# Optimization experiments

Measured on AMD Instinct MI355X. Metric: run time of the kernel, lower is better.

The kernel has to match this reference:

```python
import jax, jax.numpy as jnp
import numpy as np

# Active hierarchy constraints from the default 14x14 matrix:
# (2->5), (5->6), (6->7), (8->3)
_I = np.array([2, 5, 6, 8], dtype=np.int32)
_J = np.array([5, 6, 7, 3], dtype=np.int32)
BATCH = 2_000_000
NUM_CLASSES = 14


def setup_inputs() -> dict:
    key = jax.random.key(0)
    k1, = jax.random.split(key, 1)
    predictions = jax.random.uniform(k1, (BATCH, NUM_CLASSES), dtype=jnp.float32)
    return {
        "predictions": predictions,
        "temperature": jnp.float32(1.0),
        "i_idx": jnp.asarray(_I),
        "j_idx": jnp.asarray(_J),
    }


def reference(predictions, temperature, i_idx, j_idx):
    # Gather the parent/child probability columns: [batch, n_constraints]
    p_i = predictions[:, i_idx]
    p_j = predictions[:, j_idx]
    violation = jax.nn.relu(p_i - p_j)
    # mean over batch per constraint, each divided by temperature,
    # then averaged over the number of constraints (matches original loop)
    per_constraint = jnp.mean(violation * violation, axis=0) / temperature
    num_constraints = i_idx.shape[0]
    return jnp.sum(per_constraint) / num_constraints
```

## Files before the change

kernel.cpp:

```cpp
#include <hip/hip_runtime.h>


#define HCL_ROWS 2000000
#define HCL_NCOLS 14

__global__ __launch_bounds__(256) void
HierarchicalConsistencyLoss_kernel(const float* __restrict__ pred,
                                   const float* __restrict__ temp,
                                   float* __restrict__ out,
                                   int rows) {
    const int tid    = blockIdx.x * blockDim.x + threadIdx.x;
    const int stride = gridDim.x * blockDim.x;

    float acc = 0.0f;
    for (int r = tid; r < rows; r += stride) {
        const float* row = pred + (size_t)r * HCL_NCOLS;
        float2 ab = *reinterpret_cast<const float2*>(row + 2);
        float2 cd = *reinterpret_cast<const float2*>(row + 4);
        float2 ef = *reinterpret_cast<const float2*>(row + 6);
        float  g  = row[8];

        const float p2 = ab.x, p3 = ab.y;
        const float p5 = cd.y;
        const float p6 = ef.x, p7 = ef.y;
        const float p8 = g;

        float v0 = fmaxf(p2 - p5, 0.0f);
        float v1 = fmaxf(p5 - p6, 0.0f);
        float v2 = fmaxf(p6 - p7, 0.0f);
        float v3 = fmaxf(p8 - p3, 0.0f);

        acc = fmaf(v0, v0, acc);
        acc = fmaf(v1, v1, acc);
        acc = fmaf(v2, v2, acc);
        acc = fmaf(v3, v3, acc);
    }

    #pragma unroll
    for (int off = 32; off > 0; off >>= 1)
        acc += __shfl_down(acc, off, 64);

    __shared__ float wsum[4];
    const int lane = threadIdx.x & 63;
    const int wid  = threadIdx.x >> 6;
    if (lane == 0) wsum[wid] = acc;
    __syncthreads();

    if (threadIdx.x == 0) {
        float s = wsum[0] + wsum[1] + wsum[2] + wsum[3];
        float scale = 1.0f / ((float)rows * 4.0f * temp[0]);
        atomicAdd(out, s * scale);
    }
}

extern "C" void kernel_launch(void* const* d_in, const int* in_sizes, int n_in,
                              void* d_out, int out_size, void* d_ws, size_t ws_size,
                              hipStream_t stream) {
    const float* pred = (const float*)d_in[0];
    const float* temp = (const float*)d_in[1];
    float* out = (float*)d_out;

    hipMemsetAsync(out, 0, sizeof(float), stream);

    const int rows    = HCL_ROWS;
    const int threads = 256;
    const int blocks  = 2048;

    HierarchicalConsistencyLoss_kernel<<<blocks, threads, 0, stream>>>(pred, temp, out, rows);
}
```

Measured before the change: 174.8 us.

## Stage row tiles through shared memory with coalesced float4 loads

```diff
diff --git a/kernel.cpp b/kernel.cpp
--- a/kernel.cpp
+++ b/kernel.cpp
@@ -3,37 +3,47 @@
 
 #define HCL_ROWS 2000000
 #define HCL_NCOLS 14
+#define TILE_ROWS 500
+#define TILE_FLOATS (TILE_ROWS * HCL_NCOLS)
+#define TILE_VEC4 (TILE_FLOATS / 4)
+#define NTILES (HCL_ROWS / TILE_ROWS)
+#define NBLOCKS 1000
 
 __global__ __launch_bounds__(256) void
 HierarchicalConsistencyLoss_kernel(const float* __restrict__ pred,
                                    const float* __restrict__ temp,
-                                   float* __restrict__ out,
-                                   int rows) {
-    const int tid    = blockIdx.x * blockDim.x + threadIdx.x;
-    const int stride = gridDim.x * blockDim.x;
+                                   float* __restrict__ out) {
+    __shared__ float tile[TILE_FLOATS];
 
     float acc = 0.0f;
-    for (int r = tid; r < rows; r += stride) {
-        const float* row = pred + (size_t)r * HCL_NCOLS;
-        float2 ab = *reinterpret_cast<const float2*>(row + 2);
-        float2 cd = *reinterpret_cast<const float2*>(row + 4);
-        float2 ef = *reinterpret_cast<const float2*>(row + 6);
-        float  g  = row[8];
 
-        const float p2 = ab.x, p3 = ab.y;
-        const float p5 = cd.y;
-        const float p6 = ef.x, p7 = ef.y;
-        const float p8 = g;
+    for (int t = blockIdx.x; t < NTILES; t += gridDim.x) {
+        const float4* src = reinterpret_cast<const float4*>(pred + (size_t)t * TILE_FLOATS);
 
-        float v0 = fmaxf(p2 - p5, 0.0f);
-        float v1 = fmaxf(p5 - p6, 0.0f);
-        float v2 = fmaxf(p6 - p7, 0.0f);
-        float v3 = fmaxf(p8 - p3, 0.0f);
+        __syncthreads();
 
-        acc = fmaf(v0, v0, acc);
-        acc = fmaf(v1, v1, acc);
-        acc = fmaf(v2, v2, acc);
-        acc = fmaf(v3, v3, acc);
+        for (int l = threadIdx.x; l < TILE_VEC4; l += 256)
+            reinterpret_cast<float4*>(tile)[l] = src[l];
+
+        __syncthreads();
+
+        for (int r = threadIdx.x; r < TILE_ROWS; r += 256) {
+            const float* row = tile + r * HCL_NCOLS;
+            float2 ab = *reinterpret_cast<const float2*>(row + 2);
+            float  p5 = row[5];
+            float2 ef = *reinterpret_cast<const float2*>(row + 6);
+            float  p8 = row[8];
+
+            float v0 = fmaxf(ab.x - p5,  0.0f);
+            float v1 = fmaxf(p5  - ef.x, 0.0f);
+            float v2 = fmaxf(ef.x - ef.y, 0.0f);
+            float v3 = fmaxf(p8  - ab.y, 0.0f);
+
+            acc = fmaf(v0, v0, acc);
+            acc = fmaf(v1, v1, acc);
+            acc = fmaf(v2, v2, acc);
+            acc = fmaf(v3, v3, acc);
+        }
     }
 
     #pragma unroll
@@ -48,7 +58,7 @@
 
     if (threadIdx.x == 0) {
         float s = wsum[0] + wsum[1] + wsum[2] + wsum[3];
-        float scale = 1.0f / ((float)rows * 4.0f * temp[0]);
+        float scale = 1.0f / ((float)HCL_ROWS * 4.0f * temp[0]);
         atomicAdd(out, s * scale);
     }
 }
@@ -62,9 +72,5 @@
 
     hipMemsetAsync(out, 0, sizeof(float), stream);
 
-    const int rows    = HCL_ROWS;
-    const int threads = 256;
-    const int blocks  = 2048;
-
-    HierarchicalConsistencyLoss_kernel<<<blocks, threads, 0, stream>>>(pred, temp, out, rows);
+    HierarchicalConsistencyLoss_kernel<<<NBLOCKS, 256, 0, stream>>>(pred, temp, out);
 }
```

New measurement: 174.5 us. Within noise of the previous version (-0.1%).
